# Optimization experiments

Measured on AMD Instinct MI355X. Metric: run time of the kernel, lower is better.

## Reference

```python
import jax, jax.numpy as jnp
import numpy as np

N = 8192          # number of nodes (dense_shape of the sparse adjacency)
E = 262144        # number of edges (nnz of the sparse tensor), avg degree 32
FLOW_ITERS = 10   # self.flow_iters


def setup_inputs() -> dict:
    key = jax.random.key(0)
    k1, k2, k3, k4 = jax.random.split(key, 4)
    rows = jax.random.randint(k1, (E,), 0, N, dtype=jnp.int32)
    cols = jax.random.randint(k2, (E,), 0, N, dtype=jnp.int32)
    values = jax.random.uniform(k3, (E,), dtype=jnp.float32)      # sparse edge weights (proportions)
    demands = jax.random.normal(k4, (N, 1), dtype=jnp.float32)    # per-node demands
    return {"values": values, "demands": demands, "rows": rows, "cols": cols}


def reference(values, demands, rows, cols):
    d = demands[:, 0]  # [N]

    def step(flow_vals, _):
        # tf.sparse.reduce_sum(flow, axis=0): sum over rows -> per-column inflow [N]
        inflow = jax.ops.segment_sum(flow_vals, cols, num_segments=N)
        # relu(inflow[:, None] - demands) -> per-node adjusted inflow [N]
        adj = jax.nn.relu(inflow - d)
        # sparse * dense with [N,1] broadcast: scale each edge by adj of its row
        return values * adj[rows], None

    flow0 = jnp.zeros_like(values)  # initial empty sparse flow == all-zero values
    flow, _ = jax.lax.scan(step, flow0, None, length=FLOW_ITERS)

    # tf.sparse.to_dense(flow)
    return jnp.zeros((N, N), dtype=values.dtype).at[rows, cols].add(flow)
```

## Files before the change

### kernel.cpp

```cpp
#include <hip/hip_runtime.h>


#define NN 8192
#define EE 262144
#define THREADS 1024
#define SORTB 32
#define EPB (EE / SORTB)
#define NB 256
#define CPB (NN / NB)
#define GROWS 32
#define NBLK 256
#define MAGIC 0x5CA1AB1Eu

typedef unsigned long long u64;

#define LOAD_AU(p)    __hip_atomic_load((p),  __ATOMIC_RELAXED, __HIP_MEMORY_SCOPE_AGENT)
#define STORE_AU(p,v) __hip_atomic_store((p), (v), __ATOMIC_RELAXED, __HIP_MEMORY_SCOPE_AGENT)

#define LBAR() do { asm volatile("s_waitcnt lgkmcnt(0)" ::: "memory"); \
                    __builtin_amdgcn_s_barrier(); \
                    __builtin_amdgcn_sched_barrier(0); } while (0)

union SM {
    struct { unsigned cnt[SORTB * NB]; unsigned hist[NB]; unsigned bst[NB + 1]; unsigned offs[NB]; } so;
    struct { float acc[CPB]; float dem[CPB]; } c;
    struct { float img[2 * NN]; u64 eL[2048]; } s;
    char pad[90112];
};

__device__ __forceinline__ void flag_barrier_n(unsigned* fl, int idx, int tid, int nblk) {
    if (tid == 0) STORE_AU(&fl[idx], MAGIC);
    asm volatile("" ::: "memory");
    if (tid < 64) {
        for (;;) {
            unsigned f = (tid < nblk) ? LOAD_AU(&fl[tid]) : MAGIC;
            if (__all(f == MAGIC)) break;
            __builtin_amdgcn_s_sleep(2);
        }
    }
    asm volatile("" ::: "memory");
    __syncthreads();
}

__device__ __forceinline__ void flag_barrier_256(unsigned* fl, int idx, int tid) {
    if (tid == 0) STORE_AU(&fl[idx], MAGIC);
    asm volatile("" ::: "memory");
    if (tid < 64) {
        for (;;) {
            unsigned a = LOAD_AU(&fl[tid]);
            unsigned b = LOAD_AU(&fl[tid + 64]);
            unsigned c = LOAD_AU(&fl[tid + 128]);
            unsigned d = LOAD_AU(&fl[tid + 192]);
            if (__all(a == MAGIC && b == MAGIC && c == MAGIC && d == MAGIC)) break;
            __builtin_amdgcn_s_sleep(2);
        }
    }
    asm volatile("" ::: "memory");
    __syncthreads();
}

template <int SLP>
__device__ __forceinline__ void wait_flags_n(unsigned* fl, int tid, int nblk) {
    if (tid < 64) {
        for (;;) {
            unsigned f = (tid < nblk) ? LOAD_AU(&fl[tid]) : MAGIC;
            if (__all(f == MAGIC)) break;
            __builtin_amdgcn_s_sleep(SLP);
        }
    }
    asm volatile("" ::: "memory");
    __syncthreads();
}

__global__ void __launch_bounds__(THREADS) mega(
        const float* __restrict__ values, const float* __restrict__ dem,
        const int* __restrict__ rows, const int* __restrict__ cols,
        u64* __restrict__ se,
        u64* __restrict__ se2,
        float* __restrict__ adjF,
        float* __restrict__ adj9f,
        unsigned* __restrict__ cnt,
        unsigned* __restrict__ cnt2,
        unsigned* __restrict__ bstart,
        unsigned* __restrict__ gstart,
        unsigned* __restrict__ flagsC, unsigned* __restrict__ flagsR,
        unsigned* __restrict__ flagsE, unsigned* __restrict__ flagsR2,
        unsigned* __restrict__ flagsK,
        float* __restrict__ out) {
    __shared__ SM sm;
    __shared__ float a9[GROWS];
    const int bid = blockIdx.x, tid = threadIdx.x;

    if (bid < SORTB) {
        if (tid < NB) sm.so.hist[tid] = 0;
        __syncthreads();
        const int4* c4 = (const int4*)(cols + bid * EPB);
        int4 ca = c4[2 * tid], cb = c4[2 * tid + 1];
        atomicAdd(&sm.so.hist[ca.x >> 5], 1u);  atomicAdd(&sm.so.hist[ca.y >> 5], 1u);
        atomicAdd(&sm.so.hist[ca.z >> 5], 1u);  atomicAdd(&sm.so.hist[ca.w >> 5], 1u);
        atomicAdd(&sm.so.hist[cb.x >> 5], 1u);  atomicAdd(&sm.so.hist[cb.y >> 5], 1u);
        atomicAdd(&sm.so.hist[cb.z >> 5], 1u);  atomicAdd(&sm.so.hist[cb.w >> 5], 1u);
        __syncthreads();
        if (tid < NB) STORE_AU(&cnt[bid * NB + tid], sm.so.hist[tid]);
        __syncthreads();
        flag_barrier_n(flagsC, bid, tid, SORTB);

        #pragma unroll
        for (int j = 0; j < (SORTB * NB) / THREADS; ++j)
            sm.so.cnt[tid + j * THREADS] = LOAD_AU(&cnt[tid + j * THREADS]);
        __syncthreads();
        if (tid < NB) {
            unsigned t = 0;
            for (int b = 0; b < SORTB; ++b) t += sm.so.cnt[b * NB + tid];
            sm.so.hist[tid] = t;
        }
        __syncthreads();
        if (tid == 0) {
            unsigned run = 0;
            for (int k = 0; k < NB; ++k) { sm.so.bst[k] = run; run += sm.so.hist[k]; }
            sm.so.bst[NB] = run;
        }
        __syncthreads();
        if (tid < NB) {
            unsigned off = sm.so.bst[tid];
            for (int b = 0; b < bid; ++b) off += sm.so.cnt[b * NB + tid];
            sm.so.offs[tid] = off;
        }
        if (bid == 0 && tid <= NB) STORE_AU(&bstart[tid], sm.so.bst[tid]);
        __syncthreads();

        {
            const int4*   r4 = (const int4*)(rows + bid * EPB);
            const float4* v4 = (const float4*)(values + bid * EPB);
            int4 ra = r4[2 * tid], rb = r4[2 * tid + 1];
            float4 va = v4[2 * tid], vb = v4[2 * tid + 1];
            #define PUSHC(R, C, V) do {                                        \
                unsigned dst_ = atomicAdd(&sm.so.offs[(C) >> 5], 1u);          \
                u64 w_ = (unsigned)((R) | (((C) & 31) << 13))                  \
                       | ((u64)__float_as_uint(V) << 32);                      \
                STORE_AU(&se[dst_], w_);                                       \
            } while (0)
            PUSHC(ra.x, ca.x, va.x);  PUSHC(ra.y, ca.y, va.y);
            PUSHC(ra.z, ca.z, va.z);  PUSHC(ra.w, ca.w, va.w);
            PUSHC(rb.x, cb.x, vb.x);  PUSHC(rb.y, cb.y, vb.y);
            PUSHC(rb.z, cb.z, vb.z);  PUSHC(rb.w, cb.w, vb.w);
            #undef PUSHC
        }
        __syncthreads();
        flag_barrier_n(flagsE, bid, tid, SORTB);
    } else if (bid < 2 * SORTB) {
        const int b2 = bid - SORTB;
        if (tid < NB) sm.so.hist[tid] = 0;
        __syncthreads();
        const int4* r4 = (const int4*)(rows + b2 * EPB);
        int4 ra = r4[2 * tid], rb = r4[2 * tid + 1];
        atomicAdd(&sm.so.hist[ra.x >> 5], 1u);  atomicAdd(&sm.so.hist[ra.y >> 5], 1u);
        atomicAdd(&sm.so.hist[ra.z >> 5], 1u);  atomicAdd(&sm.so.hist[ra.w >> 5], 1u);
        atomicAdd(&sm.so.hist[rb.x >> 5], 1u);  atomicAdd(&sm.so.hist[rb.y >> 5], 1u);
        atomicAdd(&sm.so.hist[rb.z >> 5], 1u);  atomicAdd(&sm.so.hist[rb.w >> 5], 1u);
        __syncthreads();
        if (tid < NB) STORE_AU(&cnt2[b2 * NB + tid], sm.so.hist[tid]);
        __syncthreads();
        flag_barrier_n(flagsR, b2, tid, SORTB);

        #pragma unroll
        for (int j = 0; j < (SORTB * NB) / THREADS; ++j)
            sm.so.cnt[tid + j * THREADS] = LOAD_AU(&cnt2[tid + j * THREADS]);
        __syncthreads();
        if (tid < NB) {
            unsigned t = 0;
            for (int b = 0; b < SORTB; ++b) t += sm.so.cnt[b * NB + tid];
            sm.so.hist[tid] = t;
        }
        __syncthreads();
        if (tid == 0) {
            unsigned run = 0;
            for (int k = 0; k < NB; ++k) { sm.so.bst[k] = run; run += sm.so.hist[k]; }
            sm.so.bst[NB] = run;
        }
        __syncthreads();
        if (tid < NB) {
            unsigned off = sm.so.bst[tid];
            for (int b = 0; b < b2; ++b) off += sm.so.cnt[b * NB + tid];
            sm.so.offs[tid] = off;
        }
        if (b2 == 0 && tid <= NB) STORE_AU(&gstart[tid], sm.so.bst[tid]);
        __syncthreads();

        {
            const int4*   c4 = (const int4*)(cols + b2 * EPB);
            const float4* v4 = (const float4*)(values + b2 * EPB);
            int4 ca = c4[2 * tid], cb = c4[2 * tid + 1];
            float4 va = v4[2 * tid], vb = v4[2 * tid + 1];
            #define PUSHR(R, C, V) do {                                        \
                unsigned dst_ = atomicAdd(&sm.so.offs[(R) >> 5], 1u);          \
                u64 w_ = (unsigned)((C) | (((R) & 31) << 13))                  \
                       | ((u64)__float_as_uint(V) << 32);                      \
                STORE_AU(&se2[dst_], w_);                                      \
            } while (0)
            PUSHR(ra.x, ca.x, va.x);  PUSHR(ra.y, ca.y, va.y);
            PUSHR(ra.z, ca.z, va.z);  PUSHR(ra.w, ca.w, va.w);
            PUSHR(rb.x, cb.x, vb.x);  PUSHR(rb.y, cb.y, vb.y);
            PUSHR(rb.z, cb.z, vb.z);  PUSHR(rb.w, cb.w, vb.w);
            #undef PUSHR
        }
        __syncthreads();
        if (tid == 0) STORE_AU(&flagsR2[b2], MAGIC);
        asm volatile("" ::: "memory");
        wait_flags_n<4>(flagsE, tid, SORTB);
    } else {
        wait_flags_n<8>(flagsE, tid, SORTB);
    }

    const int bs = (int)LOAD_AU(&bstart[bid]);
    const int be = (int)LOAD_AU(&bstart[bid + 1]);
    const int ne = be - bs;
    u64 e0 = 0, e1 = 0;
    if (tid < ne)           e0 = LOAD_AU(&se[bs + tid]);
    if (THREADS + tid < ne) e1 = LOAD_AU(&se[bs + THREADS + tid]);
    if (tid < CPB) sm.c.dem[tid] = dem[bid * CPB + tid];

    for (int s = 1; s <= 9; ++s) {
        if (tid < CPB) sm.c.acc[tid] = 0.f;
        __syncthreads();

        #define EDGE(W) do {                                                   \
            unsigned m_ = (unsigned)(W);                                       \
            float v_ = __uint_as_float((unsigned)((W) >> 32));                 \
            int r_ = m_ & (NN - 1);                                            \
            float a_ = (s == 1) ? fmaxf(-dem[r_], 0.f)                         \
                                : LOAD_AU(&adjF[(size_t)(s - 1) * NN + r_]);   \
            atomicAdd(&sm.c.acc[(m_ >> 13) & 31], v_ * a_);                    \
        } while (0)
        if (tid < ne)           EDGE(e0);
        if (THREADS + tid < ne) EDGE(e1);
        for (int i = bs + 2 * THREADS + tid; i < be; i += THREADS) {
            u64 w = LOAD_AU(&se[i]);
            EDGE(w);
        }
        #undef EDGE
        __syncthreads();

        if (tid < CPB) {
            float r = fmaxf(sm.c.acc[tid] - sm.c.dem[tid], 0.f);
            if (s < 9) STORE_AU(&adjF[(size_t)s * NN + bid * CPB + tid], r);
            else       STORE_AU(&adj9f[bid * CPB + tid], r);
        }
        __syncthreads();
        flag_barrier_256(flagsK + (s - 1) * NB, bid, tid);
    }
    wait_flags_n<2>(flagsR2, tid, SORTB);

    {
        const int g = bid;
        const unsigned gs = LOAD_AU(&gstart[g]), ge = LOAD_AU(&gstart[g + 1]);
        const unsigned n = ge - gs;
        const unsigned ncp = n < 2048u ? n : 2048u;
        if (tid < GROWS) a9[tid] = LOAD_AU(&adj9f[g * GROWS + tid]);
        __syncthreads();

        for (unsigned i = tid; i < ncp; i += THREADS) {
            u64 w = LOAD_AU(&se2[gs + i]);
            unsigned m = (unsigned)w;
            float v = __uint_as_float((unsigned)(w >> 32));
            sm.s.eL[i] = (u64)m | ((u64)__float_as_uint(v * a9[(m >> 13) & 31]) << 32);
        }
        __syncthreads();

        const float4 z4 = make_float4(0.f, 0.f, 0.f, 0.f);
        for (int r = 0; r < GROWS; ++r) {
            float* im = sm.s.img + (r & 1) * NN;
            ((float4*)im)[tid]        = z4;
            ((float4*)im)[tid + 1024] = z4;
            LBAR();
            for (unsigned i = tid; i < ncp; i += THREADS) {
                u64 w = sm.s.eL[i];
                unsigned m = (unsigned)w;
                if (((m >> 13) & 31) == (unsigned)r)
                    atomicAdd(&im[m & (NN - 1)], __uint_as_float((unsigned)(w >> 32)));
            }
            for (unsigned i = 2048u + tid; i < n; i += THREADS) {
                u64 w = LOAD_AU(&se2[gs + i]);
                unsigned m = (unsigned)w;
                if (((m >> 13) & 31) == (unsigned)r)
                    atomicAdd(&im[m & (NN - 1)],
                              __uint_as_float((unsigned)(w >> 32)) * a9[r]);
            }
            LBAR();
            float4 w0 = ((const float4*)im)[tid];
            float4 w1 = ((const float4*)im)[tid + 1024];
            float4* o4 = (float4*)(out + (size_t)(g * GROWS + r) * NN);
            o4[tid]        = w0;
            o4[tid + 1024] = w1;
        }
    }
}

extern "C" void kernel_launch(void* const* d_in, const int* in_sizes, int n_in,
                              void* d_out, int out_size, void* d_ws, size_t ws_size,
                              hipStream_t stream) {
    const float* values = (const float*)d_in[0];
    const float* dem    = (const float*)d_in[1];
    const int*   rows   = (const int*)d_in[2];
    const int*   cols   = (const int*)d_in[3];
    float* out = (float*)d_out;

    u64*      se      = (u64*)d_ws;
    u64*      se2     = se + (size_t)EE;
    float*    adjF    = (float*)(se2 + (size_t)EE);
    float*    adj9f   = adjF + 9L * NN;
    unsigned* cnt     = (unsigned*)(adj9f + NN);
    unsigned* cnt2    = cnt + SORTB * NB;
    unsigned* bstart  = cnt2 + SORTB * NB;
    unsigned* gstart  = bstart + 320;
    unsigned* flagsC  = gstart + 320;
    unsigned* flagsR  = flagsC + 64;
    unsigned* flagsE  = flagsR + 64;
    unsigned* flagsR2 = flagsE + 64;
    unsigned* flagsK  = flagsR2 + 64;

    mega<<<NBLK, THREADS, 0, stream>>>(
        values, dem, rows, cols, se, se2, adjF, adj9f, cnt, cnt2,
        bstart, gstart, flagsC, flagsR, flagsE, flagsR2, flagsK, out);
}
```

Baseline: 343.3 us.

## Row-bucket edges in LDS and accumulate dense output in registers

In the final densify phase, each group's edges are now bucketed by local row with an LDS counting sort. For each row, every thread then scans that row's edges and accumulates its eight owned columns in registers with compare-and-select. This replaces the double-buffered LDS image with its per-row zeroing, barriers and shared-memory atomics. Separately, the number of sort blocks is doubled so each block handles half as many edges, which adds parallelism in the bucketing phases. The trade is redundant compare work in every thread, and a serial per-thread scan of any overflow edges beyond the LDS capacity.

Measured after the change: 481.2 us. +40.2%, slower.

```diff
diff --git a/kernel.cpp b/kernel.cpp
--- a/kernel.cpp
+++ b/kernel.cpp
@@ -4,11 +4,12 @@
 #define NN 8192
 #define EE 262144
 #define THREADS 1024
-#define SORTB 32
+#define SORTB 64
 #define EPB (EE / SORTB)
 #define NB 256
 #define CPB (NN / NB)
 #define GROWS 32
+#define ECAP 2048
 #define NBLK 256
 #define MAGIC 0x5CA1AB1Eu
 
@@ -17,15 +18,12 @@
 #define LOAD_AU(p)    __hip_atomic_load((p),  __ATOMIC_RELAXED, __HIP_MEMORY_SCOPE_AGENT)
 #define STORE_AU(p,v) __hip_atomic_store((p), (v), __ATOMIC_RELAXED, __HIP_MEMORY_SCOPE_AGENT)
 
-#define LBAR() do { asm volatile("s_waitcnt lgkmcnt(0)" ::: "memory"); \
-                    __builtin_amdgcn_s_barrier(); \
-                    __builtin_amdgcn_sched_barrier(0); } while (0)
-
 union SM {
-    struct { unsigned cnt[SORTB * NB]; unsigned hist[NB]; unsigned bst[NB + 1]; unsigned offs[NB]; } so;
+    struct { unsigned cnt[SORTB * NB]; unsigned hist[NB]; unsigned bst[NB + 1];
+             unsigned offs[NB]; } so;
     struct { float acc[CPB]; float dem[CPB]; } c;
-    struct { float img[2 * NN]; u64 eL[2048]; } s;
-    char pad[90112];
+    struct { u64 eL[ECAP]; u64 eL2[ECAP]; unsigned hist[32];
+             unsigned rs[GROWS + 1]; unsigned offs[32]; } s;
 };
 
 __device__ __forceinline__ void flag_barrier_n(unsigned* fl, int idx, int tid, int nblk) {
@@ -95,11 +93,9 @@
         if (tid < NB) sm.so.hist[tid] = 0;
         __syncthreads();
         const int4* c4 = (const int4*)(cols + bid * EPB);
-        int4 ca = c4[2 * tid], cb = c4[2 * tid + 1];
+        int4 ca = c4[tid];
         atomicAdd(&sm.so.hist[ca.x >> 5], 1u);  atomicAdd(&sm.so.hist[ca.y >> 5], 1u);
         atomicAdd(&sm.so.hist[ca.z >> 5], 1u);  atomicAdd(&sm.so.hist[ca.w >> 5], 1u);
-        atomicAdd(&sm.so.hist[cb.x >> 5], 1u);  atomicAdd(&sm.so.hist[cb.y >> 5], 1u);
-        atomicAdd(&sm.so.hist[cb.z >> 5], 1u);  atomicAdd(&sm.so.hist[cb.w >> 5], 1u);
         __syncthreads();
         if (tid < NB) STORE_AU(&cnt[bid * NB + tid], sm.so.hist[tid]);
         __syncthreads();
@@ -132,8 +128,7 @@
         {
             const int4*   r4 = (const int4*)(rows + bid * EPB);
             const float4* v4 = (const float4*)(values + bid * EPB);
-            int4 ra = r4[2 * tid], rb = r4[2 * tid + 1];
-            float4 va = v4[2 * tid], vb = v4[2 * tid + 1];
+            int4 ra = r4[tid];  float4 va = v4[tid];
             #define PUSHC(R, C, V) do {                                        \
                 unsigned dst_ = atomicAdd(&sm.so.offs[(C) >> 5], 1u);          \
                 u64 w_ = (unsigned)((R) | (((C) & 31) << 13))                  \
@@ -142,8 +137,6 @@
             } while (0)
             PUSHC(ra.x, ca.x, va.x);  PUSHC(ra.y, ca.y, va.y);
             PUSHC(ra.z, ca.z, va.z);  PUSHC(ra.w, ca.w, va.w);
-            PUSHC(rb.x, cb.x, vb.x);  PUSHC(rb.y, cb.y, vb.y);
-            PUSHC(rb.z, cb.z, vb.z);  PUSHC(rb.w, cb.w, vb.w);
             #undef PUSHC
         }
         __syncthreads();
@@ -153,11 +146,9 @@
         if (tid < NB) sm.so.hist[tid] = 0;
         __syncthreads();
         const int4* r4 = (const int4*)(rows + b2 * EPB);
-        int4 ra = r4[2 * tid], rb = r4[2 * tid + 1];
+        int4 ra = r4[tid];
         atomicAdd(&sm.so.hist[ra.x >> 5], 1u);  atomicAdd(&sm.so.hist[ra.y >> 5], 1u);
         atomicAdd(&sm.so.hist[ra.z >> 5], 1u);  atomicAdd(&sm.so.hist[ra.w >> 5], 1u);
-        atomicAdd(&sm.so.hist[rb.x >> 5], 1u);  atomicAdd(&sm.so.hist[rb.y >> 5], 1u);
-        atomicAdd(&sm.so.hist[rb.z >> 5], 1u);  atomicAdd(&sm.so.hist[rb.w >> 5], 1u);
         __syncthreads();
         if (tid < NB) STORE_AU(&cnt2[b2 * NB + tid], sm.so.hist[tid]);
         __syncthreads();
@@ -190,8 +181,7 @@
         {
             const int4*   c4 = (const int4*)(cols + b2 * EPB);
             const float4* v4 = (const float4*)(values + b2 * EPB);
-            int4 ca = c4[2 * tid], cb = c4[2 * tid + 1];
-            float4 va = v4[2 * tid], vb = v4[2 * tid + 1];
+            int4 ca = c4[tid];  float4 va = v4[tid];
             #define PUSHR(R, C, V) do {                                        \
                 unsigned dst_ = atomicAdd(&sm.so.offs[(R) >> 5], 1u);          \
                 u64 w_ = (unsigned)((C) | (((R) & 31) << 13))                  \
@@ -200,8 +190,6 @@
             } while (0)
             PUSHR(ra.x, ca.x, va.x);  PUSHR(ra.y, ca.y, va.y);
             PUSHR(ra.z, ca.z, va.z);  PUSHR(ra.w, ca.w, va.w);
-            PUSHR(rb.x, cb.x, vb.x);  PUSHR(rb.y, cb.y, vb.y);
-            PUSHR(rb.z, cb.z, vb.z);  PUSHR(rb.w, cb.w, vb.w);
             #undef PUSHR
         }
         __syncthreads();
@@ -255,43 +243,65 @@
         const int g = bid;
         const unsigned gs = LOAD_AU(&gstart[g]), ge = LOAD_AU(&gstart[g + 1]);
         const unsigned n = ge - gs;
-        const unsigned ncp = n < 2048u ? n : 2048u;
+        const unsigned ncp = n < (unsigned)ECAP ? n : (unsigned)ECAP;
         if (tid < GROWS) a9[tid] = LOAD_AU(&adj9f[g * GROWS + tid]);
         __syncthreads();
 
         for (unsigned i = tid; i < ncp; i += THREADS) {
             u64 w = LOAD_AU(&se2[gs + i]);
             unsigned m = (unsigned)w;
-            float v = __uint_as_float((unsigned)(w >> 32));
-            sm.s.eL[i] = (u64)m | ((u64)__float_as_uint(v * a9[(m >> 13) & 31]) << 32);
-        }
-        __syncthreads();
-
-        const float4 z4 = make_float4(0.f, 0.f, 0.f, 0.f);
+            float v = __uint_as_float((unsigned)(w >> 32)) * a9[(m >> 13) & 31];
+            sm.s.eL[i] = (u64)m | ((u64)__float_as_uint(v) << 32);
+        }
+        if (tid < 32) sm.s.hist[tid] = 0;
+        __syncthreads();
+        for (unsigned i = tid; i < ncp; i += THREADS)
+            atomicAdd(&sm.s.hist[((unsigned)sm.s.eL[i] >> 13) & 31], 1u);
+        __syncthreads();
+        if (tid == 0) {
+            unsigned run = 0;
+            for (int k = 0; k < 32; ++k) { sm.s.rs[k] = run; run += sm.s.hist[k]; }
+            sm.s.rs[32] = run;
+        }
+        __syncthreads();
+        if (tid < 32) sm.s.offs[tid] = sm.s.rs[tid];
+        __syncthreads();
+        for (unsigned i = tid; i < ncp; i += THREADS) {
+            u64 w = sm.s.eL[i];
+            unsigned dst = atomicAdd(&sm.s.offs[((unsigned)w >> 13) & 31], 1u);
+            sm.s.eL2[dst] = w;
+        }
+        __syncthreads();
+
+        const int cb0 = 4 * tid, cb1 = 4096 + 4 * tid;
         for (int r = 0; r < GROWS; ++r) {
-            float* im = sm.s.img + (r & 1) * NN;
-            ((float4*)im)[tid]        = z4;
-            ((float4*)im)[tid + 1024] = z4;
-            LBAR();
-            for (unsigned i = tid; i < ncp; i += THREADS) {
-                u64 w = sm.s.eL[i];
-                unsigned m = (unsigned)w;
-                if (((m >> 13) & 31) == (unsigned)r)
-                    atomicAdd(&im[m & (NN - 1)], __uint_as_float((unsigned)(w >> 32)));
+            float x0 = 0.f, x1 = 0.f, x2 = 0.f, x3 = 0.f;
+            float y0 = 0.f, y1 = 0.f, y2 = 0.f, y3 = 0.f;
+            const unsigned s0 = sm.s.rs[r], s1 = sm.s.rs[r + 1];
+            for (unsigned i = s0; i < s1; ++i) {
+                u64 w = sm.s.eL2[i];
+                int c = (int)((unsigned)w & (NN - 1));
+                float v = __uint_as_float((unsigned)(w >> 32));
+                x0 += (c == cb0)     ? v : 0.f;  x1 += (c == cb0 + 1) ? v : 0.f;
+                x2 += (c == cb0 + 2) ? v : 0.f;  x3 += (c == cb0 + 3) ? v : 0.f;
+                y0 += (c == cb1)     ? v : 0.f;  y1 += (c == cb1 + 1) ? v : 0.f;
+                y2 += (c == cb1 + 2) ? v : 0.f;  y3 += (c == cb1 + 3) ? v : 0.f;
             }
-            for (unsigned i = 2048u + tid; i < n; i += THREADS) {
+            for (unsigned i = ECAP; i < n; ++i) {
                 u64 w = LOAD_AU(&se2[gs + i]);
                 unsigned m = (unsigned)w;
-                if (((m >> 13) & 31) == (unsigned)r)
-                    atomicAdd(&im[m & (NN - 1)],
-                              __uint_as_float((unsigned)(w >> 32)) * a9[r]);
+                if (((m >> 13) & 31) == (unsigned)r) {
+                    int c = (int)(m & (NN - 1));
+                    float v = __uint_as_float((unsigned)(w >> 32)) * a9[r];
+                    x0 += (c == cb0)     ? v : 0.f;  x1 += (c == cb0 + 1) ? v : 0.f;
+                    x2 += (c == cb0 + 2) ? v : 0.f;  x3 += (c == cb0 + 3) ? v : 0.f;
+                    y0 += (c == cb1)     ? v : 0.f;  y1 += (c == cb1 + 1) ? v : 0.f;
+                    y2 += (c == cb1 + 2) ? v : 0.f;  y3 += (c == cb1 + 3) ? v : 0.f;
+                }
             }
-            LBAR();
-            float4 w0 = ((const float4*)im)[tid];
-            float4 w1 = ((const float4*)im)[tid + 1024];
             float4* o4 = (float4*)(out + (size_t)(g * GROWS + r) * NN);
-            o4[tid]        = w0;
-            o4[tid + 1024] = w1;
+            o4[tid]        = make_float4(x0, x1, x2, x3);
+            o4[tid + 1024] = make_float4(y0, y1, y2, y3);
         }
     }
 }
```
